# Kernel optimization log

Measured on AMD Instinct MI355X. Metric: run time of the kernel, lower is better.

Reference implementation:

```python
import jax, jax.numpy as jnp
import numpy as np

NUM_ITERATIONS = 3


def setup_inputs() -> dict:
    key = jax.random.key(0)
    k1, k2 = jax.random.split(key)
    B, I, C, U, D = 64, 8, 2048, 32, 16
    x = jax.random.normal(k1, (B, I, C), dtype=jnp.float32)
    # W matches torch param (1, C, U, D, I) with leading 1 squeezed
    W = jax.random.normal(k2, (C, U, D, I), dtype=jnp.float32)
    return {"x": x, "W": W}


def _squash(s):
    # Faithful to the original: reduction over axis 1 of s (B, U, D),
    # which corresponds to dim=2 of the torch tensor (B, 1, U, D, 1)
    # i.e. the num_units axis (quirk of the original code, reproduced).
    mag_sq = jnp.sum(s * s, axis=1, keepdims=True)  # (B, 1, D)
    mag = jnp.sqrt(mag_sq)
    return mag_sq / (1.0 + mag_sq) * (s / mag)


def reference(x, W):
    # x: (B, in_units, in_channels); W: (C, U, D, I)
    B = x.shape[0]
    x_t = jnp.transpose(x, (0, 2, 1))  # (B, C, I)
    # u_hat[b,c,u,d] = sum_i W[c,u,d,i] * x_t[b,c,i]
    u_hat = jnp.einsum("bci,cudi->bcud", x_t, W)  # (B, C, U, D)
    b_ij = jnp.zeros(W.shape[:2], dtype=u_hat.dtype)  # (C, U)
    v = None
    for _ in range(NUM_ITERATIONS):
        c_ij = jax.nn.softmax(b_ij, axis=1)  # softmax over num_units
        s_j = jnp.einsum("cu,bcud->bud", c_ij, u_hat)  # (B, U, D)
        v = _squash(s_j)  # (B, U, D)
        # agreement: dot over D, mean over batch -> (C, U)
        b_ij = b_ij + jnp.einsum("bcud,bud->cu", u_hat, v) / B
    # torch returns v_j.squeeze(1): shape (B, U, D, 1)
    return v[..., None]
```

## Files before the change

### kernel.cpp

```cpp
#include <hip/hip_runtime.h>

typedef __attribute__((ext_vector_type(8))) short short8;
typedef __attribute__((ext_vector_type(4))) float f32x4;

__device__ __forceinline__ unsigned int f2bf1(float f) {
    union { float f; unsigned int u; } v; v.f = f;
    return (v.u + 0x7fffu + ((v.u >> 16) & 1u)) >> 16;
}
__device__ __forceinline__ unsigned int packbf(float a, float b) {
    return f2bf1(a) | (f2bf1(b) << 16);
}
__device__ __forceinline__ float bf1(unsigned short h) {
    union { unsigned int u; float f; } v; v.u = ((unsigned int)h) << 16;
    return v.f;
}

__global__ __launch_bounds__(256) void transpose_kernel(const float* __restrict__ x,
                                                        float* __restrict__ xt,
                                                        unsigned short* __restrict__ x2b) {
    __shared__ float tile[64][65];
    const int bi0 = (blockIdx.x >> 5) << 6;
    const int c0  = (blockIdx.x & 31) << 6;
    const int tx = threadIdx.x & 63, ty = threadIdx.x >> 6;
#pragma unroll
    for (int p = 0; p < 16; ++p)
        tile[ty + p * 4][tx] = x[(size_t)(bi0 + ty + p * 4) * 2048 + c0 + tx];
    __syncthreads();
#pragma unroll
    for (int p = 0; p < 16; ++p) {
        const int c = c0 + ty + p * 4;
        const int bi = bi0 + tx;
        const float val = tile[tx][ty + p * 4];
        xt[(size_t)c * 512 + bi] = val;
        x2b[(size_t)c * 512 + (bi & 7) * 64 + (bi >> 3)] = (unsigned short)f2bf1(val);
    }
}

__global__ __launch_bounds__(256) void softmax_kernel(const float* __restrict__ bij,
                                                      float* __restrict__ cij) {
    int c = blockIdx.x * 256 + threadIdx.x;
    float vals[32];
    float m = -1e30f;
#pragma unroll
    for (int u = 0; u < 32; ++u) { vals[u] = bij[c * 32 + u]; m = fmaxf(m, vals[u]); }
    float ssum = 0.f;
#pragma unroll
    for (int u = 0; u < 32; ++u) { vals[u] = expf(vals[u] - m); ssum += vals[u]; }
    float inv = 1.f / ssum;
#pragma unroll
    for (int u = 0; u < 32; ++u) cij[c * 32 + u] = vals[u] * inv;
}

template <int UNIFORM, int MODE>
__global__ __launch_bounds__(256) void smfma_kernel(const float* __restrict__ xt,
                                                    const float* __restrict__ W,
                                                    unsigned short* __restrict__ Wb,
                                                    const float* __restrict__ cij,
                                                    float* __restrict__ part) {
    const int chunk = blockIdx.x >> 5;
    const int u     = blockIdx.x & 31;
    const int t = threadIdx.x, w = t >> 6, l = t & 63;
    const int m  = l & 15;
    const int kb = l >> 4;
    const int b  = w * 16 + m;

    f32x4 acc = {0.f, 0.f, 0.f, 0.f};
    const int c00 = chunk * 32;

#pragma unroll 4
    for (int q = 0; q < 8; ++q) {
        const int c = c00 + q * 4 + kb;
        const size_t wofs = ((size_t)c * 32 + u) * 128 + m * 8;
        uint4 av;
        if (MODE == 1) {
            const float4* Wp = reinterpret_cast<const float4*>(W + wofs);
            float4 w0 = Wp[0], w1 = Wp[1];
            av.x = packbf(w0.x, w0.y); av.y = packbf(w0.z, w0.w);
            av.z = packbf(w1.x, w1.y); av.w = packbf(w1.z, w1.w);
            if (w == 0) *reinterpret_cast<uint4*>(Wb + wofs) = av;
        } else {
            av = *reinterpret_cast<const uint4*>(Wb + wofs);
        }
        const float4* xp = reinterpret_cast<const float4*>(xt + ((size_t)c * 64 + b) * 8);
        float4 x0 = xp[0], x1 = xp[1];
        const float cw = UNIFORM ? 0.03125f : cij[c * 32 + u];
        uint4 bv;
        bv.x = packbf(x0.x * cw, x0.y * cw);
        bv.y = packbf(x0.z * cw, x0.w * cw);
        bv.z = packbf(x1.x * cw, x1.y * cw);
        bv.w = packbf(x1.z * cw, x1.w * cw);
        acc = __builtin_amdgcn_mfma_f32_16x16x32_bf16(
            __builtin_bit_cast(short8, av), __builtin_bit_cast(short8, bv), acc, 0, 0, 0);
    }

    *reinterpret_cast<f32x4*>(part + (size_t)blockIdx.x * 1024 + t * 4) = acc;
}

__global__ __launch_bounds__(256) void reduce_kernel(const float* __restrict__ part,
                                                     float* __restrict__ s) {
    const int tid = blockIdx.x * 256 + threadIdx.x;
    const int u = tid >> 8, w = (tid >> 6) & 3, lane = tid & 63;
    const float4* p = reinterpret_cast<const float4*>(part) + ((size_t)u * 256 + w * 64 + lane);
    float4 a = p[0];
#pragma unroll
    for (int k = 1; k < 64; ++k) {
        float4 q = p[(size_t)k * 8192];
        a.x += q.x; a.y += q.y; a.z += q.z; a.w += q.w;
    }
    const float* ap = &a.x;
    const int bcol = w * 16 + (lane & 15);
#pragma unroll
    for (int r = 0; r < 4; ++r) {
        const int d = (lane >> 4) * 4 + r;
        s[((size_t)u * 16 + d) * 64 + bcol] = ap[r];
    }
}

__global__ __launch_bounds__(256) void v_kernel3(const float* __restrict__ s,
                                                 float* __restrict__ out,
                                                 unsigned short* __restrict__ vTb) {
    int n = blockIdx.x * 256 + threadIdx.x;
    int b = n >> 4, d = n & 15;
    float sv[32];
    float msq = 0.f;
#pragma unroll
    for (int u = 0; u < 32; ++u) {
        sv[u] = s[(u * 16 + d) * 64 + b];
        msq += sv[u] * sv[u];
    }
    float scale = msq / ((1.f + msq) * sqrtf(msq));
#pragma unroll
    for (int u = 0; u < 32; ++u) {
        float val = sv[u] * scale;
        out[(b * 32 + u) * 16 + d] = val;
        vTb[((size_t)u * 16 + d) * 64 + b] = (unsigned short)f2bf1(val);
    }
}

template <int FIRST>
__global__ __launch_bounds__(256) void delta_mfma(const unsigned short* __restrict__ x2b,
                                                  const unsigned short* __restrict__ Wb,
                                                  const unsigned short* __restrict__ vTb,
                                                  float* __restrict__ bij) {
    const int cg = blockIdx.x >> 5;
    const int u  = blockIdx.x & 31;
    const int t = threadIdx.x, w = t >> 6, l = t & 63;
    const int m = l & 15, kb = l >> 4;
    const int ci = m & 7;
    const int chalf = m >> 3;

    const uint4 a0 = *reinterpret_cast<const uint4*>(vTb + ((size_t)u * 16 + m) * 64 + kb * 8);
    const uint4 a1 = *reinterpret_cast<const uint4*>(vTb + ((size_t)u * 16 + m) * 64 + 32 + kb * 8);

#pragma unroll 2
    for (int j = 0; j < 8; ++j) {
        const int cpair = cg * 32 + w * 8 + j;
        const int c = cpair * 2 + chalf;
        const uint4 b0 = *reinterpret_cast<const uint4*>(x2b + (size_t)c * 512 + ci * 64 + kb * 8);
        const uint4 b1 = *reinterpret_cast<const uint4*>(x2b + (size_t)c * 512 + ci * 64 + 32 + kb * 8);
        f32x4 acc = {0.f, 0.f, 0.f, 0.f};
        acc = __builtin_amdgcn_mfma_f32_16x16x32_bf16(
            __builtin_bit_cast(short8, a0), __builtin_bit_cast(short8, b0), acc, 0, 0, 0);
        acc = __builtin_amdgcn_mfma_f32_16x16x32_bf16(
            __builtin_bit_cast(short8, a1), __builtin_bit_cast(short8, b1), acc, 0, 0, 0);
        float dot = 0.f;
#pragma unroll
        for (int r = 0; r < 4; ++r) {
            const int d = kb * 4 + r;
            dot += acc[r] * bf1(Wb[((size_t)c * 32 + u) * 128 + d * 8 + ci]);
        }
        dot += __shfl_xor(dot, 16);
        dot += __shfl_xor(dot, 32);
        dot += __shfl_xor(dot, 1);
        dot += __shfl_xor(dot, 2);
        dot += __shfl_xor(dot, 4);
        if (l == 0 || l == 8) {
            const int cc = cpair * 2 + (l >> 3);
            float r = dot * (1.0f / 64.0f);
            if (!FIRST) r += bij[cc * 32 + u];
            bij[cc * 32 + u] = r;
        }
    }
}

extern "C" void kernel_launch(void* const* d_in, const int* in_sizes, int n_in,
                              void* d_out, int out_size, void* d_ws, size_t ws_size,
                              hipStream_t stream) {
    const float* x = (const float*)d_in[0];
    const float* W = (const float*)d_in[1];
    float* out = (float*)d_out;

    float* ws   = (float*)d_ws;
    float* xt   = ws;
    float* part = xt + 1048576;
    float* bij  = part + 2097152;
    float* cij  = bij + 65536;
    float* s    = cij + 65536;
    unsigned short* Wb  = (unsigned short*)(s + 32768);
    unsigned short* x2b = Wb + 8388608;
    unsigned short* vTb = x2b + 1048576;

    transpose_kernel<<<256, 256, 0, stream>>>(x, xt, x2b);

    smfma_kernel<1, 1><<<2048, 256, 0, stream>>>(xt, W, Wb, cij, part);
    reduce_kernel<<<32, 256, 0, stream>>>(part, s);
    v_kernel3<<<4, 256, 0, stream>>>(s, out, vTb);
    delta_mfma<1><<<1024, 256, 0, stream>>>(x2b, Wb, vTb, bij);
    softmax_kernel<<<8, 256, 0, stream>>>(bij, cij);

    smfma_kernel<0, 2><<<2048, 256, 0, stream>>>(xt, W, Wb, cij, part);
    reduce_kernel<<<32, 256, 0, stream>>>(part, s);
    v_kernel3<<<4, 256, 0, stream>>>(s, out, vTb);
    delta_mfma<0><<<1024, 256, 0, stream>>>(x2b, Wb, vTb, bij);
    softmax_kernel<<<8, 256, 0, stream>>>(bij, cij);

    smfma_kernel<0, 2><<<2048, 256, 0, stream>>>(xt, W, Wb, cij, part);
    reduce_kernel<<<32, 256, 0, stream>>>(part, s);
    v_kernel3<<<4, 256, 0, stream>>>(s, out, vTb);
}
```

Before: 194.4 us.

## Fold softmax coefficients into bf16 W copy and store x in bf16

Replaces the per-row softmax kernel with a kernel that computes softmax per channel and writes a scaled bf16 copy of W (Wcb). The s_j MFMA kernel then reads pre-scaled W and pre-converted bf16 x directly, so it no longer loads fp32 x or does per-element scaling and packing. It also splits the accumulator into two MFMA chains and fully unrolls the loop. In exchange, each iteration reads and writes the full 16 MB bf16 W an extra time, adds a second rounding of the scaled weights, and uses extra workspace.

```diff
diff --git a/kernel.cpp b/kernel.cpp
--- a/kernel.cpp
+++ b/kernel.cpp
@@ -14,9 +14,14 @@
     union { unsigned int u; float f; } v; v.u = ((unsigned int)h) << 16;
     return v.f;
 }
+__device__ __forceinline__ unsigned int scale2(unsigned int p, float s) {
+    float lo = bf1((unsigned short)(p & 0xffffu)) * s;
+    float hi = bf1((unsigned short)(p >> 16)) * s;
+    return packbf(lo, hi);
+}
 
 __global__ __launch_bounds__(256) void transpose_kernel(const float* __restrict__ x,
-                                                        float* __restrict__ xt,
+                                                        unsigned short* __restrict__ xbb,
                                                         unsigned short* __restrict__ x2b) {
     __shared__ float tile[64][65];
     const int bi0 = (blockIdx.x >> 5) << 6;
@@ -30,32 +35,48 @@
     for (int p = 0; p < 16; ++p) {
         const int c = c0 + ty + p * 4;
         const int bi = bi0 + tx;
-        const float val = tile[tx][ty + p * 4];
-        xt[(size_t)c * 512 + bi] = val;
-        x2b[(size_t)c * 512 + (bi & 7) * 64 + (bi >> 3)] = (unsigned short)f2bf1(val);
-    }
-}
-
-__global__ __launch_bounds__(256) void softmax_kernel(const float* __restrict__ bij,
-                                                      float* __restrict__ cij) {
-    int c = blockIdx.x * 256 + threadIdx.x;
-    float vals[32];
-    float m = -1e30f;
-#pragma unroll
-    for (int u = 0; u < 32; ++u) { vals[u] = bij[c * 32 + u]; m = fmaxf(m, vals[u]); }
-    float ssum = 0.f;
-#pragma unroll
-    for (int u = 0; u < 32; ++u) { vals[u] = expf(vals[u] - m); ssum += vals[u]; }
-    float inv = 1.f / ssum;
-#pragma unroll
-    for (int u = 0; u < 32; ++u) cij[c * 32 + u] = vals[u] * inv;
+        const unsigned short h = (unsigned short)f2bf1(tile[tx][ty + p * 4]);
+        xbb[(size_t)c * 512 + bi] = h;
+        x2b[(size_t)c * 512 + (bi & 7) * 64 + (bi >> 3)] = h;
+    }
+}
+
+__global__ __launch_bounds__(256) void smws_kernel(const float* __restrict__ bij,
+                                                   const unsigned short* __restrict__ Wb,
+                                                   unsigned short* __restrict__ Wcb) {
+    const int c = blockIdx.x;
+    const int t = threadIdx.x;
+    __shared__ float sm[32];
+    if (t < 32) {
+        float val = bij[c * 32 + t];
+        float mx = val;
+#pragma unroll
+        for (int mask = 16; mask >= 1; mask >>= 1) mx = fmaxf(mx, __shfl_xor(mx, mask));
+        float e = expf(val - mx);
+        float ssum = e;
+#pragma unroll
+        for (int mask = 16; mask >= 1; mask >>= 1) ssum += __shfl_xor(ssum, mask);
+        sm[t] = e / ssum;
+    }
+    __syncthreads();
+#pragma unroll
+    for (int j = 0; j < 2; ++j) {
+        const int r = t * 2 + j;
+        const float scale = sm[r >> 4];
+        const size_t ofs = (size_t)c * 4096 + r * 8;
+        uint4 h = *reinterpret_cast<const uint4*>(Wb + ofs);
+        uint4 o;
+        o.x = scale2(h.x, scale); o.y = scale2(h.y, scale);
+        o.z = scale2(h.z, scale); o.w = scale2(h.w, scale);
+        *reinterpret_cast<uint4*>(Wcb + ofs) = o;
+    }
 }
 
 template <int UNIFORM, int MODE>
-__global__ __launch_bounds__(256) void smfma_kernel(const float* __restrict__ xt,
+__global__ __launch_bounds__(256) void smfma_kernel(const unsigned short* __restrict__ xbb,
                                                     const float* __restrict__ W,
                                                     unsigned short* __restrict__ Wb,
-                                                    const float* __restrict__ cij,
+                                                    const unsigned short* __restrict__ WA,
                                                     float* __restrict__ part) {
     const int chunk = blockIdx.x >> 5;
     const int u     = blockIdx.x & 31;
@@ -64,10 +85,10 @@
     const int kb = l >> 4;
     const int b  = w * 16 + m;
 
-    f32x4 acc = {0.f, 0.f, 0.f, 0.f};
+    f32x4 acc0 = {0.f, 0.f, 0.f, 0.f}, acc1 = {0.f, 0.f, 0.f, 0.f};
     const int c00 = chunk * 32;
 
-#pragma unroll 4
+#pragma unroll
     for (int q = 0; q < 8; ++q) {
         const int c = c00 + q * 4 + kb;
         const size_t wofs = ((size_t)c * 32 + u) * 128 + m * 8;
@@ -79,20 +100,19 @@
             av.z = packbf(w1.x, w1.y); av.w = packbf(w1.z, w1.w);
             if (w == 0) *reinterpret_cast<uint4*>(Wb + wofs) = av;
         } else {
-            av = *reinterpret_cast<const uint4*>(Wb + wofs);
+            av = *reinterpret_cast<const uint4*>(WA + wofs);
         }
-        const float4* xp = reinterpret_cast<const float4*>(xt + ((size_t)c * 64 + b) * 8);
-        float4 x0 = xp[0], x1 = xp[1];
-        const float cw = UNIFORM ? 0.03125f : cij[c * 32 + u];
-        uint4 bv;
-        bv.x = packbf(x0.x * cw, x0.y * cw);
-        bv.y = packbf(x0.z * cw, x0.w * cw);
-        bv.z = packbf(x1.x * cw, x1.y * cw);
-        bv.w = packbf(x1.z * cw, x1.w * cw);
-        acc = __builtin_amdgcn_mfma_f32_16x16x32_bf16(
-            __builtin_bit_cast(short8, av), __builtin_bit_cast(short8, bv), acc, 0, 0, 0);
-    }
-
+        const uint4 bv = *reinterpret_cast<const uint4*>(xbb + ((size_t)c * 64 + b) * 8);
+        if (q & 1)
+            acc1 = __builtin_amdgcn_mfma_f32_16x16x32_bf16(
+                __builtin_bit_cast(short8, av), __builtin_bit_cast(short8, bv), acc1, 0, 0, 0);
+        else
+            acc0 = __builtin_amdgcn_mfma_f32_16x16x32_bf16(
+                __builtin_bit_cast(short8, av), __builtin_bit_cast(short8, bv), acc0, 0, 0, 0);
+    }
+
+    f32x4 acc = acc0 + acc1;
+    if (UNIFORM) acc *= 0.03125f;
     *reinterpret_cast<f32x4*>(part + (size_t)blockIdx.x * 1024 + t * 4) = acc;
 }
 
@@ -191,30 +211,30 @@
     float* out = (float*)d_out;
 
     float* ws   = (float*)d_ws;
-    float* xt   = ws;
-    float* part = xt + 1048576;
+    float* part = ws;
     float* bij  = part + 2097152;
-    float* cij  = bij + 65536;
-    float* s    = cij + 65536;
+    float* s    = bij + 65536;
     unsigned short* Wb  = (unsigned short*)(s + 32768);
-    unsigned short* x2b = Wb + 8388608;
+    unsigned short* Wcb = Wb + 8388608;
+    unsigned short* xbb = Wcb + 8388608;
+    unsigned short* x2b = xbb + 1048576;
     unsigned short* vTb = x2b + 1048576;
 
-    transpose_kernel<<<256, 256, 0, stream>>>(x, xt, x2b);
-
-    smfma_kernel<1, 1><<<2048, 256, 0, stream>>>(xt, W, Wb, cij, part);
+    transpose_kernel<<<256, 256, 0, stream>>>(x, xbb, x2b);
+
+    smfma_kernel<1, 1><<<2048, 256, 0, stream>>>(xbb, W, Wb, Wb, part);
     reduce_kernel<<<32, 256, 0, stream>>>(part, s);
     v_kernel3<<<4, 256, 0, stream>>>(s, out, vTb);
     delta_mfma<1><<<1024, 256, 0, stream>>>(x2b, Wb, vTb, bij);
-    softmax_kernel<<<8, 256, 0, stream>>>(bij, cij);
-
-    smfma_kernel<0, 2><<<2048, 256, 0, stream>>>(xt, W, Wb, cij, part);
+
+    smws_kernel<<<2048, 256, 0, stream>>>(bij, Wb, Wcb);
+    smfma_kernel<0, 2><<<2048, 256, 0, stream>>>(xbb, W, Wb, Wcb, part);
     reduce_kernel<<<32, 256, 0, stream>>>(part, s);
     v_kernel3<<<4, 256, 0, stream>>>(s, out, vTb);
     delta_mfma<0><<<1024, 256, 0, stream>>>(x2b, Wb, vTb, bij);
-    softmax_kernel<<<8, 256, 0, stream>>>(bij, cij);
-
-    smfma_kernel<0, 2><<<2048, 256, 0, stream>>>(xt, W, Wb, cij, part);
+
+    smws_kernel<<<2048, 256, 0, stream>>>(bij, Wb, Wcb);
+    smfma_kernel<0, 2><<<2048, 256, 0, stream>>>(xbb, W, Wb, Wcb, part);
     reduce_kernel<<<32, 256, 0, stream>>>(part, s);
     v_kernel3<<<4, 256, 0, stream>>>(s, out, vTb);
 }
```

Result: faster. 187.6 us (-3.5%).
